# Kernel tuning notes

Hardware: AMD Instinct MI355X
Metric: run time of the kernel (lower is better)

Reference implementation:

```python
import jax, jax.numpy as jnp
import numpy as np

B, N, F_NUM, H_NUM = 2, 8192, 64, 64


def _linear_params(key, fan_in, fan_out, bias=True):
    k1, k2 = jax.random.split(key)
    bound = 1.0 / np.sqrt(fan_in)
    W = jax.random.uniform(k1, (fan_in, fan_out), minval=-bound, maxval=bound, dtype=jnp.float32)
    if bias:
        b = jax.random.uniform(k2, (fan_out,), minval=-bound, maxval=bound, dtype=jnp.float32)
        return W, b
    return W


def setup_inputs() -> dict:
    key = jax.random.key(0)
    ks = jax.random.split(key, 12)
    Wk, bk = _linear_params(ks[0], F_NUM, H_NUM)
    Wa, ba = _linear_params(ks[1], H_NUM, F_NUM)
    Wq = _linear_params(ks[2], H_NUM, H_NUM, bias=False)
    Wks = _linear_params(ks[3], H_NUM, H_NUM, bias=False)
    Wv = _linear_params(ks[4], H_NUM, H_NUM, bias=False)
    Wp1, bp1 = _linear_params(ks[5], 4, H_NUM)
    Wp2, bp2 = _linear_params(ks[6], H_NUM, H_NUM)
    Wt1, bt1 = _linear_params(ks[7], H_NUM, H_NUM)
    Wt2, bt2 = _linear_params(ks[8], H_NUM, H_NUM)
    xyzp = jax.random.normal(ks[9], (B, N, 4), dtype=jnp.float32)
    features = jax.random.normal(ks[10], (B, N, F_NUM), dtype=jnp.float32)
    return dict(xyzp=xyzp, features=features, Wk=Wk, bk=bk, Wq=Wq, Wks=Wks, Wv=Wv,
                Wp1=Wp1, bp1=bp1, Wp2=Wp2, bp2=bp2, Wt1=Wt1, bt1=bt1, Wt2=Wt2, bt2=bt2,
                Wa=Wa, ba=ba, k_nearest=16)


def _knn_idx(xyz, K):
    sq = jnp.sum(xyz * xyz, axis=-1)                      # [B,N]
    d = sq[:, :, None] + sq[:, None, :] - 2.0 * jnp.einsum('bnd,bmd->bnm', xyz, xyz)
    _, idx = jax.lax.top_k(-d, K)                         # [B,N,K] nearest (incl. self)
    return idx


def _knn_gather(x, idx):
    # x: [B,N,C], idx: [B,N,K] -> [B,N,K,C]
    return jax.vmap(lambda xb, ib: xb[ib])(x, idx)


def reference(xyzp, features, Wk, bk, Wq, Wks, Wv, Wp1, bp1, Wp2, bp2,
              Wt1, bt1, Wt2, bt2, Wa, ba, k_nearest):
    xyz = xyzp[:, :, :3]
    idx = _knn_idx(xyz, k_nearest)                        # [B,N,K]
    # positional encoding MLP on relative xyzp
    rel = xyzp[:, :, None, :] - _knn_gather(xyzp, idx)    # [B,N,K,4]
    pos_enc = jax.nn.relu(rel @ Wp1 + bp1) @ Wp2 + bp2    # [B,N,K,H]
    x = features @ Wk + bk                                # [B,N,H]
    q = x @ Wq                                            # [B,N,H]
    k = _knn_gather(x @ Wks, idx)                         # [B,N,K,H]
    v = _knn_gather(x @ Wv, idx)                          # [B,N,K,H]
    a_in = q[:, :, None, :] - k + pos_enc                 # [B,N,K,H]
    attn = jax.nn.relu(a_in @ Wt1 + bt1) @ Wt2 + bt2      # [B,N,K,H]
    attn = jax.nn.softmax(attn / np.sqrt(H_NUM).astype(np.float32), axis=-2)
    res = jnp.einsum('bnkh,bnkh->bnh', attn, v + pos_enc) # per-channel weighted sum over K
    return res @ Wa + ba + features
```

## Files before the change

kernel.cpp:

```cpp
#include <hip/hip_runtime.h>

#define NPTS 8192
#define HDIM 64
#define KNN 16
#define LOG2E 1.4426950408889634f

typedef __attribute__((ext_vector_type(8))) short bf8_t;
typedef __attribute__((ext_vector_type(4))) float f4_t;
#define MFMA16(a, b, c) __builtin_amdgcn_mfma_f32_16x16x32_bf16(a, b, c, 0, 0, 0)

__device__ __forceinline__ float fast_exp(float x) {
    float y = x * LOG2E;
    float r;
    asm volatile("v_exp_f32 %0, %1\n\ts_nop 1" : "=v"(r) : "v"(y));
    return r;
}
__device__ __forceinline__ unsigned short f2b(float x) {
    unsigned v = __float_as_uint(x);
    return (unsigned short)((v + 0x7FFFu + ((v >> 16) & 1u)) >> 16);
}

#define OFF_QW   0u
#define OFF_KW   (4u << 20)
#define OFF_VW   (8u << 20)
#define OFF_FRAG (12u << 20)
#define OFF_KNN  ((12u << 20) + 32768u)

__global__ void prefrag_kernel(const float* __restrict__ Wp2,
                               const float* __restrict__ Wt1,
                               const float* __restrict__ Wt2,
                               unsigned short* __restrict__ dst)
{
    int i = blockIdx.x * 256 + threadIdx.x;
    if (i >= 3 * 4096) return;
    int st = i >> 12, e = i & 4095;
    const float* W = (st == 0) ? Wp2 : (st == 1) ? Wt1 : Wt2;
    int k = e >> 6, n = e & 63;
    int s = k >> 5, quad = (k >> 3) & 3, j = k & 7;
    int t = n >> 4, l = quad * 16 + (n & 15);
    dst[st * 4096 + (s * 4 + t) * 512 + l * 8 + j] = f2b(W[e]);
}

__global__ __launch_bounds__(1024) void proj_kernel(
    const float* __restrict__ feat,
    const float* __restrict__ Wk, const float* __restrict__ bk,
    const float* __restrict__ Wq, const float* __restrict__ Wks,
    const float* __restrict__ Wv,
    float* __restrict__ qw, float* __restrict__ kw, float* __restrict__ vw)
{
    __shared__ __align__(16) float4 sW[4][1024];
    int tid = threadIdx.x;
    sW[0][tid] = ((const float4*)Wk)[tid];
    sW[1][tid] = ((const float4*)Wq)[tid];
    sW[2][tid] = ((const float4*)Wks)[tid];
    sW[3][tid] = ((const float4*)Wv)[tid];
    __syncthreads();
    const float* sWk  = (const float*)sW[0];
    const float* sWq  = (const float*)sW[1];
    const float* sWks = (const float*)sW[2];
    const float* sWv  = (const float*)sW[3];

    int w = tid >> 6, lane = tid & 63;
    int p = blockIdx.x * 16 + w;
    float f = feat[(size_t)p * HDIM + lane];
    float x = bk[lane];
    #pragma unroll 8
    for (int c = 0; c < 64; ++c) x += __shfl(f, c) * sWk[c * 64 + lane];
    float q = 0.f, k = 0.f, v = 0.f;
    #pragma unroll 8
    for (int c = 0; c < 64; ++c) {
        float xc = __shfl(x, c);
        q += xc * sWq[c * 64 + lane];
        k += xc * sWks[c * 64 + lane];
        v += xc * sWv[c * 64 + lane];
    }
    qw[(size_t)p * HDIM + lane] = q;
    kw[(size_t)p * HDIM + lane] = k;
    vw[(size_t)p * HDIM + lane] = v;
}

__global__ __launch_bounds__(256) void knn4_kernel(
    const float* __restrict__ xyzp, int* __restrict__ knnIdx)
{
    int w = threadIdx.x >> 6, lane = threadIdx.x & 63;
    int wid = blockIdx.x * 4 + w;
    int pbase = wid * 4;
    int b = pbase >> 13;
    int nbase = pbase & (NPTS - 1);
    const float4* xb4 = (const float4*)xyzp + (size_t)b * NPTS;

    float qx[4], qy[4], qz[4], qs[4];
    #pragma unroll
    for (int qi = 0; qi < 4; ++qi) {
        float4 s = xb4[nbase + qi];
        qx[qi] = s.x; qy[qi] = s.y; qz[qi] = s.z;
        qs[qi] = s.x * s.x + s.y * s.y + s.z * s.z;
    }

    float dh[4][4]; int ih[4][4];
    #pragma unroll
    for (int qi = 0; qi < 4; ++qi)
        #pragma unroll
        for (int j = 0; j < 4; ++j) { dh[qi][j] = 3.4e38f; ih[qi][j] = 0x7fffffff; }

    for (int t = 0; t < NPTS / 256; ++t) {
        float4 c[4];
        #pragma unroll
        for (int u = 0; u < 4; ++u)
            c[u] = xb4[(t * 4 + u) * 64 + lane];
        #pragma unroll
        for (int u = 0; u < 4; ++u) {
            int m = (t * 4 + u) * 64 + lane;
            float cs = c[u].x * c[u].x + c[u].y * c[u].y + c[u].z * c[u].z;
            #pragma unroll
            for (int qi = 0; qi < 4; ++qi) {
                float d = qs[qi] + cs
                        - 2.0f * (qx[qi] * c[u].x + qy[qi] * c[u].y + qz[qi] * c[u].z);
                if (d < dh[qi][3]) {
                    dh[qi][3] = d; ih[qi][3] = m;
                    #pragma unroll
                    for (int j = 3; j >= 1; --j)
                        if (dh[qi][j] < dh[qi][j - 1]) {
                            float td = dh[qi][j]; dh[qi][j] = dh[qi][j - 1]; dh[qi][j - 1] = td;
                            int ti = ih[qi][j]; ih[qi][j] = ih[qi][j - 1]; ih[qi][j - 1] = ti;
                        }
                }
            }
        }
    }

    #pragma unroll
    for (int qi = 0; qi < 4; ++qi) {
        int mynb = 0, head = 0;
        #pragma unroll 1
        for (int r = 0; r < KNN; ++r) {
            float d = dh[qi][0]; int i = ih[qi][0];
            #pragma unroll
            for (int s = 1; s < 64; s <<= 1) {
                float d2 = __shfl_xor(d, s); int i2 = __shfl_xor(i, s);
                if (d2 < d || (d2 == d && i2 < i)) { d = d2; i = i2; }
            }
            if (lane == r) mynb = i;
            if (ih[qi][0] == i) {
                dh[qi][0] = dh[qi][1]; ih[qi][0] = ih[qi][1];
                dh[qi][1] = dh[qi][2]; ih[qi][1] = ih[qi][2];
                dh[qi][2] = dh[qi][3]; ih[qi][2] = ih[qi][3];
                dh[qi][3] = 3.4e38f; ih[qi][3] = 0x7fffffff;
                ++head;
            }
        }
        if (__any(head >= 4)) {
            float eh[16]; int ei[16];
            #pragma unroll
            for (int j = 0; j < 16; ++j) { eh[j] = 3.4e38f; ei[j] = 0x7fffffff; }
            for (int t = 0; t < NPTS / 64; ++t) {
                int m = t * 64 + lane;
                float4 c4 = xb4[m];
                float cs = c4.x * c4.x + c4.y * c4.y + c4.z * c4.z;
                float d = qs[qi] + cs
                        - 2.0f * (qx[qi] * c4.x + qy[qi] * c4.y + qz[qi] * c4.z);
                if (d < eh[15]) {
                    eh[15] = d; ei[15] = m;
                    #pragma unroll
                    for (int j = 15; j >= 1; --j)
                        if (eh[j] < eh[j - 1]) {
                            float td = eh[j]; eh[j] = eh[j - 1]; eh[j - 1] = td;
                            int ti = ei[j]; ei[j] = ei[j - 1]; ei[j - 1] = ti;
                        }
                }
            }
            #pragma unroll 1
            for (int r = 0; r < KNN; ++r) {
                float d = eh[0]; int i = ei[0];
                #pragma unroll
                for (int s = 1; s < 64; s <<= 1) {
                    float d2 = __shfl_xor(d, s); int i2 = __shfl_xor(i, s);
                    if (d2 < d || (d2 == d && i2 < i)) { d = d2; i = i2; }
                }
                if (lane == r) mynb = i;
                if (ei[0] == i) {
                    #pragma unroll
                    for (int j = 0; j < 15; ++j) { eh[j] = eh[j + 1]; ei[j] = ei[j + 1]; }
                    eh[15] = 3.4e38f; ei[15] = 0x7fffffff;
                }
            }
        }
        mynb = min(max(mynb, 0), NPTS - 1);
        if (lane < KNN) knnIdx[(size_t)(pbase + qi) * KNN + lane] = mynb;
    }
}

__global__ __launch_bounds__(256) void LocalTransformer_80513456931527_kernel(
    const float* __restrict__ xyzp, const float* __restrict__ features,
    const float* __restrict__ Wp1,  const float* __restrict__ bp1,
    const float* __restrict__ bp2,  const float* __restrict__ bt1,
    const float* __restrict__ bt2,
    const float* __restrict__ Wa,   const float* __restrict__ ba,
    const float* __restrict__ qw, const float* __restrict__ kw,
    const float* __restrict__ vw,
    const unsigned short* __restrict__ fragw,
    const int* __restrict__ knnIdx,
    float* __restrict__ out)
{
    __shared__ __align__(16) float sBounce[4][16 * 68 + 4];

    int tid = threadIdx.x, w = tid >> 6, lane = tid & 63;
    int p = blockIdx.x * 4 + w;
    int b = p >> 13;
    float* bb = sBounce[w];

    int quad = lane >> 4, l15 = lane & 15;
    int mynb = knnIdx[(size_t)p * KNN + l15];
    mynb = min(max(mynb, 0), NPTS - 1);
    int nb_a = mynb;
    int nbm[4];
    #pragma unroll
    for (int r = 0; r < 4; ++r) nbm[r] = __shfl(mynb, quad * 4 + r);

    const float4 xq4 = *(const float4*)(xyzp + (size_t)p * 4);
    const float4 xn4 = *(const float4*)(xyzp + ((size_t)b * NPTS + nb_a) * 4);
    float rel0 = xq4.x - xn4.x, rel1 = xq4.y - xn4.y;
    float rel2 = xq4.z - xn4.z, rel3 = xq4.w - xn4.w;

    bf8_t pe1f[2];
    #pragma unroll
    for (int s = 0; s < 2; ++s) {
        int hb = s * 32 + quad * 8;
        float W0[8], W1[8], W2[8], W3[8], Bb[8];
        *(float4*)&W0[0] = *(const float4*)(Wp1 +       hb);
        *(float4*)&W0[4] = *(const float4*)(Wp1 +       hb + 4);
        *(float4*)&W1[0] = *(const float4*)(Wp1 +  64 + hb);
        *(float4*)&W1[4] = *(const float4*)(Wp1 +  64 + hb + 4);
        *(float4*)&W2[0] = *(const float4*)(Wp1 + 128 + hb);
        *(float4*)&W2[4] = *(const float4*)(Wp1 + 128 + hb + 4);
        *(float4*)&W3[0] = *(const float4*)(Wp1 + 192 + hb);
        *(float4*)&W3[4] = *(const float4*)(Wp1 + 192 + hb + 4);
        *(float4*)&Bb[0] = *(const float4*)(bp1 + hb);
        *(float4*)&Bb[4] = *(const float4*)(bp1 + hb + 4);
        #pragma unroll
        for (int j = 0; j < 8; ++j) {
            float a = Bb[j] + rel0 * W0[j] + rel1 * W1[j]
                            + rel2 * W2[j] + rel3 * W3[j];
            pe1f[s][j] = (short)f2b(fmaxf(a, 0.f));
        }
    }

    const bf8_t* BW = (const bf8_t*)fragw;
    f4_t pe2c[4];
    #pragma unroll
    for (int t = 0; t < 4; ++t) {
        f4_t acc = {0.f, 0.f, 0.f, 0.f};
        acc = MFMA16(pe1f[0], BW[0 * 512 + (0 * 4 + t) * 64 + lane], acc);
        acc = MFMA16(pe1f[1], BW[0 * 512 + (1 * 4 + t) * 64 + lane], acc);
        float bias = bp2[t * 16 + l15];
        #pragma unroll
        for (int r = 0; r < 4; ++r) acc[r] += bias;
        pe2c[t] = acc;
    }

    f4_t ainc[4], vpec[4];
    #pragma unroll
    for (int t = 0; t < 4; ++t) {
        float qv = qw[(size_t)p * HDIM + t * 16 + l15];
        #pragma unroll
        for (int r = 0; r < 4; ++r) {
            size_t nbo = ((size_t)b * NPTS + nbm[r]) * HDIM + t * 16 + l15;
            ainc[t][r] = qv - kw[nbo] + pe2c[t][r];
            vpec[t][r] = vw[nbo] + pe2c[t][r];
        }
    }

    #pragma unroll
    for (int t = 0; t < 4; ++t)
        #pragma unroll
        for (int r = 0; r < 4; ++r)
            bb[(quad * 4 + r) * 68 + t * 16 + l15] = ainc[t][r];
    asm volatile("s_waitcnt lgkmcnt(0)" ::: "memory");
    bf8_t af[2];
    #pragma unroll
    for (int s = 0; s < 2; ++s) {
        float tmp[8];
        *(float4*)&tmp[0] = *(const float4*)&bb[l15 * 68 + s * 32 + quad * 8];
        *(float4*)&tmp[4] = *(const float4*)&bb[l15 * 68 + s * 32 + quad * 8 + 4];
        #pragma unroll
        for (int j = 0; j < 8; ++j) af[s][j] = (short)f2b(tmp[j]);
    }

    f4_t t1c[4];
    #pragma unroll
    for (int t = 0; t < 4; ++t) {
        f4_t acc = {0.f, 0.f, 0.f, 0.f};
        acc = MFMA16(af[0], BW[1 * 512 + (0 * 4 + t) * 64 + lane], acc);
        acc = MFMA16(af[1], BW[1 * 512 + (1 * 4 + t) * 64 + lane], acc);
        float bias = bt1[t * 16 + l15];
        #pragma unroll
        for (int r = 0; r < 4; ++r) t1c[t][r] = fmaxf(acc[r] + bias, 0.f);
    }

    asm volatile("s_waitcnt lgkmcnt(0)" ::: "memory");
    #pragma unroll
    for (int t = 0; t < 4; ++t)
        #pragma unroll
        for (int r = 0; r < 4; ++r)
            bb[(quad * 4 + r) * 68 + t * 16 + l15] = t1c[t][r];
    asm volatile("s_waitcnt lgkmcnt(0)" ::: "memory");
    bf8_t tf[2];
    #pragma unroll
    for (int s = 0; s < 2; ++s) {
        float tmp[8];
        *(float4*)&tmp[0] = *(const float4*)&bb[l15 * 68 + s * 32 + quad * 8];
        *(float4*)&tmp[4] = *(const float4*)&bb[l15 * 68 + s * 32 + quad * 8 + 4];
        #pragma unroll
        for (int j = 0; j < 8; ++j) tf[s][j] = (short)f2b(tmp[j]);
    }

    f4_t lgc[4];
    #pragma unroll
    for (int t = 0; t < 4; ++t) {
        f4_t acc = {0.f, 0.f, 0.f, 0.f};
        acc = MFMA16(tf[0], BW[2 * 512 + (0 * 4 + t) * 64 + lane], acc);
        acc = MFMA16(tf[1], BW[2 * 512 + (1 * 4 + t) * 64 + lane], acc);
        float bias = bt2[t * 16 + l15];
        #pragma unroll
        for (int r = 0; r < 4; ++r) lgc[t][r] = (acc[r] + bias) * 0.125f;
    }

    float res[4];
    #pragma unroll
    for (int t = 0; t < 4; ++t) {
        float m0 = fmaxf(fmaxf(lgc[t][0], lgc[t][1]), fmaxf(lgc[t][2], lgc[t][3]));
        m0 = fmaxf(m0, __shfl_xor(m0, 16));
        m0 = fmaxf(m0, __shfl_xor(m0, 32));
        float e0 = fast_exp(lgc[t][0] - m0), e1 = fast_exp(lgc[t][1] - m0);
        float e2 = fast_exp(lgc[t][2] - m0), e3 = fast_exp(lgc[t][3] - m0);
        float sl = e0 + e1 + e2 + e3;
        float rl = e0 * vpec[t][0] + e1 * vpec[t][1]
                 + e2 * vpec[t][2] + e3 * vpec[t][3];
        sl += __shfl_xor(sl, 16); sl += __shfl_xor(sl, 32);
        rl += __shfl_xor(rl, 16); rl += __shfl_xor(rl, 32);
        res[t] = rl / sl;
    }

    float rh = (quad == 0) ? res[0] : (quad == 1) ? res[1]
             : (quad == 2) ? res[2] : res[3];
    float f = features[(size_t)p * HDIM + lane];
    float o = ba[lane];
    #pragma unroll 8
    for (int c = 0; c < 64; ++c) o += __shfl(rh, c) * Wa[c * 64 + lane];
    out[(size_t)p * HDIM + lane] = o + f;
}

extern "C" void kernel_launch(void* const* d_in, const int* in_sizes, int n_in,
                              void* d_out, int out_size, void* d_ws, size_t ws_size,
                              hipStream_t stream)
{
    (void)in_sizes; (void)n_in; (void)out_size; (void)ws_size;
    const float* xyzp     = (const float*)d_in[0];
    const float* features = (const float*)d_in[1];
    const float* Wk  = (const float*)d_in[2];
    const float* bk  = (const float*)d_in[3];
    const float* Wq  = (const float*)d_in[4];
    const float* Wks = (const float*)d_in[5];
    const float* Wv  = (const float*)d_in[6];
    const float* Wp1 = (const float*)d_in[7];
    const float* bp1 = (const float*)d_in[8];
    const float* Wp2 = (const float*)d_in[9];
    const float* bp2 = (const float*)d_in[10];
    const float* Wt1 = (const float*)d_in[11];
    const float* bt1 = (const float*)d_in[12];
    const float* Wt2 = (const float*)d_in[13];
    const float* bt2 = (const float*)d_in[14];
    const float* Wa  = (const float*)d_in[15];
    const float* ba  = (const float*)d_in[16];
    float* out = (float*)d_out;
    char* ws = (char*)d_ws;

    float* qw = (float*)(ws + OFF_QW);
    float* kw = (float*)(ws + OFF_KW);
    float* vw = (float*)(ws + OFF_VW);
    unsigned short* fragw = (unsigned short*)(ws + OFF_FRAG);
    int* knnIdx = (int*)(ws + OFF_KNN);

    prefrag_kernel<<<48, 256, 0, stream>>>(Wp2, Wt1, Wt2, fragw);
    proj_kernel<<<(2 * NPTS) / 16, 1024, 0, stream>>>(
        features, Wk, bk, Wq, Wks, Wv, qw, kw, vw);
    knn4_kernel<<<(2 * NPTS) / 16, 256, 0, stream>>>(xyzp, knnIdx);
    LocalTransformer_80513456931527_kernel<<<(2 * NPTS) / 4, 256, 0, stream>>>(
        xyzp, features, Wp1, bp1, bp2, bt1, bt2, Wa, ba,
        qw, kw, vw, fragw, knnIdx, out);
}
```

Measured before the change: 377.4 us.

## Rewrite KNN as branchless per-lane min-max top-4 plus threshold rescan

```diff
diff --git a/kernel.cpp b/kernel.cpp
--- a/kernel.cpp
+++ b/kernel.cpp
@@ -79,30 +79,31 @@
     vw[(size_t)p * HDIM + lane] = v;
 }
 
-__global__ __launch_bounds__(256) void knn4_kernel(
+__global__ __launch_bounds__(256) void knn2_kernel(
     const float* __restrict__ xyzp, int* __restrict__ knnIdx)
 {
     int w = threadIdx.x >> 6, lane = threadIdx.x & 63;
     int wid = blockIdx.x * 4 + w;
-    int pbase = wid * 4;
+    int pbase = wid * 2;
     int b = pbase >> 13;
     int nbase = pbase & (NPTS - 1);
     const float4* xb4 = (const float4*)xyzp + (size_t)b * NPTS;
 
-    float qx[4], qy[4], qz[4], qs[4];
-    #pragma unroll
-    for (int qi = 0; qi < 4; ++qi) {
+    float qx[2], qy[2], qz[2], qs[2];
+    #pragma unroll
+    for (int qi = 0; qi < 2; ++qi) {
         float4 s = xb4[nbase + qi];
         qx[qi] = s.x; qy[qi] = s.y; qz[qi] = s.z;
         qs[qi] = s.x * s.x + s.y * s.y + s.z * s.z;
     }
 
-    float dh[4][4]; int ih[4][4];
-    #pragma unroll
-    for (int qi = 0; qi < 4; ++qi)
-        #pragma unroll
-        for (int j = 0; j < 4; ++j) { dh[qi][j] = 3.4e38f; ih[qi][j] = 0x7fffffff; }
-
+    float dh[2][4];
+    #pragma unroll
+    for (int qi = 0; qi < 2; ++qi)
+        #pragma unroll
+        for (int j = 0; j < 4; ++j) dh[qi][j] = 3.4e38f;
+
+    #pragma unroll 1
     for (int t = 0; t < NPTS / 256; ++t) {
         float4 c[4];
         #pragma unroll
@@ -110,51 +111,66 @@
             c[u] = xb4[(t * 4 + u) * 64 + lane];
         #pragma unroll
         for (int u = 0; u < 4; ++u) {
-            int m = (t * 4 + u) * 64 + lane;
             float cs = c[u].x * c[u].x + c[u].y * c[u].y + c[u].z * c[u].z;
             #pragma unroll
-            for (int qi = 0; qi < 4; ++qi) {
+            for (int qi = 0; qi < 2; ++qi) {
                 float d = qs[qi] + cs
                         - 2.0f * (qx[qi] * c[u].x + qy[qi] * c[u].y + qz[qi] * c[u].z);
-                if (d < dh[qi][3]) {
-                    dh[qi][3] = d; ih[qi][3] = m;
+                float b1 = fmaxf(dh[qi][0], d);  dh[qi][0] = fminf(dh[qi][0], d);
+                float b2 = fmaxf(dh[qi][1], b1); dh[qi][1] = fminf(dh[qi][1], b1);
+                float b3 = fmaxf(dh[qi][2], b2); dh[qi][2] = fminf(dh[qi][2], b2);
+                dh[qi][3] = fminf(dh[qi][3], b3);
+            }
+        }
+    }
+
+    #pragma unroll
+    for (int qi = 0; qi < 2; ++qi) {
+        float thr = 3.4e38f;
+        #pragma unroll 1
+        for (int r = 0; r < KNN; ++r) {
+            float dmin = dh[qi][0];
+            #pragma unroll
+            for (int s = 1; s < 64; s <<= 1)
+                dmin = fminf(dmin, __shfl_xor(dmin, s));
+            if (r == KNN - 1) thr = dmin;
+            if (dh[qi][0] == dmin) {
+                dh[qi][0] = dh[qi][1]; dh[qi][1] = dh[qi][2];
+                dh[qi][2] = dh[qi][3]; dh[qi][3] = 3.4e38f;
+            }
+        }
+
+        float eh[16]; int ei[16];
+        #pragma unroll
+        for (int j = 0; j < 16; ++j) { eh[j] = 3.4e38f; ei[j] = 0x7fffffff; }
+        int cnt = 0;
+        #pragma unroll 1
+        for (int t2 = 0; t2 < NPTS / 64; ++t2) {
+            int m = t2 * 64 + lane;
+            float4 c4 = xb4[m];
+            float cs = c4.x * c4.x + c4.y * c4.y + c4.z * c4.z;
+            float d = qs[qi] + cs
+                    - 2.0f * (qx[qi] * c4.x + qy[qi] * c4.y + qz[qi] * c4.z);
+            if (d <= thr) {
+                ++cnt;
+                if (d < eh[15]) {
+                    eh[15] = d; ei[15] = m;
                     #pragma unroll
-                    for (int j = 3; j >= 1; --j)
-                        if (dh[qi][j] < dh[qi][j - 1]) {
-                            float td = dh[qi][j]; dh[qi][j] = dh[qi][j - 1]; dh[qi][j - 1] = td;
-                            int ti = ih[qi][j]; ih[qi][j] = ih[qi][j - 1]; ih[qi][j - 1] = ti;
+                    for (int j = 15; j >= 1; --j)
+                        if (eh[j] < eh[j - 1]) {
+                            float td = eh[j]; eh[j] = eh[j - 1]; eh[j - 1] = td;
+                            int ti = ei[j]; ei[j] = ei[j - 1]; ei[j - 1] = ti;
                         }
                 }
             }
         }
-    }
-
-    #pragma unroll
-    for (int qi = 0; qi < 4; ++qi) {
-        int mynb = 0, head = 0;
-        #pragma unroll 1
-        for (int r = 0; r < KNN; ++r) {
-            float d = dh[qi][0]; int i = ih[qi][0];
-            #pragma unroll
-            for (int s = 1; s < 64; s <<= 1) {
-                float d2 = __shfl_xor(d, s); int i2 = __shfl_xor(i, s);
-                if (d2 < d || (d2 == d && i2 < i)) { d = d2; i = i2; }
-            }
-            if (lane == r) mynb = i;
-            if (ih[qi][0] == i) {
-                dh[qi][0] = dh[qi][1]; ih[qi][0] = ih[qi][1];
-                dh[qi][1] = dh[qi][2]; ih[qi][1] = ih[qi][2];
-                dh[qi][2] = dh[qi][3]; ih[qi][2] = ih[qi][3];
-                dh[qi][3] = 3.4e38f; ih[qi][3] = 0x7fffffff;
-                ++head;
-            }
-        }
-        if (__any(head >= 4)) {
-            float eh[16]; int ei[16];
+
+        int mynb = 0;
+        if (__any(cnt > 16)) {
             #pragma unroll
             for (int j = 0; j < 16; ++j) { eh[j] = 3.4e38f; ei[j] = 0x7fffffff; }
-            for (int t = 0; t < NPTS / 64; ++t) {
-                int m = t * 64 + lane;
+            for (int t2 = 0; t2 < NPTS / 64; ++t2) {
+                int m = t2 * 64 + lane;
                 float4 c4 = xb4[m];
                 float cs = c4.x * c4.x + c4.y * c4.y + c4.z * c4.z;
                 float d = qs[qi] + cs
@@ -169,20 +185,20 @@
                         }
                 }
             }
-            #pragma unroll 1
-            for (int r = 0; r < KNN; ++r) {
-                float d = eh[0]; int i = ei[0];
+        }
+        #pragma unroll 1
+        for (int r = 0; r < KNN; ++r) {
+            float d = eh[0]; int i = ei[0];
+            #pragma unroll
+            for (int s = 1; s < 64; s <<= 1) {
+                float d2 = __shfl_xor(d, s); int i2 = __shfl_xor(i, s);
+                if (d2 < d || (d2 == d && i2 < i)) { d = d2; i = i2; }
+            }
+            if (lane == r) mynb = i;
+            if (ei[0] == i) {
                 #pragma unroll
-                for (int s = 1; s < 64; s <<= 1) {
-                    float d2 = __shfl_xor(d, s); int i2 = __shfl_xor(i, s);
-                    if (d2 < d || (d2 == d && i2 < i)) { d = d2; i = i2; }
-                }
-                if (lane == r) mynb = i;
-                if (ei[0] == i) {
-                    #pragma unroll
-                    for (int j = 0; j < 15; ++j) { eh[j] = eh[j + 1]; ei[j] = ei[j + 1]; }
-                    eh[15] = 3.4e38f; ei[15] = 0x7fffffff;
-                }
+                for (int j = 0; j < 15; ++j) { eh[j] = eh[j + 1]; ei[j] = ei[j + 1]; }
+                eh[15] = 3.4e38f; ei[15] = 0x7fffffff;
             }
         }
         mynb = min(max(mynb, 0), NPTS - 1);
@@ -384,7 +400,7 @@
     prefrag_kernel<<<48, 256, 0, stream>>>(Wp2, Wt1, Wt2, fragw);
     proj_kernel<<<(2 * NPTS) / 16, 1024, 0, stream>>>(
         features, Wk, bk, Wq, Wks, Wv, qw, kw, vw);
-    knn4_kernel<<<(2 * NPTS) / 16, 256, 0, stream>>>(xyzp, knnIdx);
+    knn2_kernel<<<(2 * NPTS) / 8, 256, 0, stream>>>(xyzp, knnIdx);
     LocalTransformer_80513456931527_kernel<<<(2 * NPTS) / 4, 256, 0, stream>>>(
         xyzp, features, Wp1, bp1, bp2, bt1, bt2, Wa, ba,
         qw, kw, vw, fragw, knnIdx, out);
```

Measured after the change: 380.7 us. Within noise of the previous version (+0.9%).
